# Kernel tuning notes

Measured on AMD Instinct MI355X. Metric: run time of the kernel, lower is better.

Reference implementation:

```python
import jax, jax.numpy as jnp
import numpy as np

OUT, IN = 4096, 4096
B, S = 2, 2048

def setup_inputs() -> dict:
    key = jax.random.key(0)
    k1, k2, k3, k4 = jax.random.split(key, 4)
    x = jax.random.normal(k1, (B, S, IN), dtype=jnp.float32)
    # symmetric int8 quantized weight [out, in]
    weight_q = jax.random.randint(k2, (OUT, IN), -128, 128, dtype=jnp.int32).astype(jnp.int8)
    # per-output-channel scale, small positive (like |w|_max/127)
    scale = (jax.random.uniform(k3, (1, OUT), dtype=jnp.float32) * 0.01 + 1e-4)
    bias = jax.random.normal(k4, (OUT,), dtype=jnp.float32)
    return {"x": x, "weight_q": weight_q, "scale": scale, "bias": bias}

def reference(x, weight_q, scale, bias):
    # out = (x_2d @ W_q^T (dequantized)) * scale + bias
    x2d = x.reshape(-1, x.shape[-1])                       # [B*S, in]
    w = weight_q.astype(x.dtype)                            # dequant cast [out, in]
    out = jnp.einsum('ni,oi->no', x2d, w) * scale           # [B*S, out] * [1, out]
    out = out.reshape(x.shape[:-1] + (out.shape[-1],))
    return out + bias
```

## Files before the change

kernel.cpp:

```cpp
#include <hip/hip_runtime.h>
#include <stdint.h>


#define M_DIM 4096
#define N_DIM 4096
#define K_DIM 4096
#define BM 128
#define BN 256
#define BK 32
#define KT_N (K_DIM / BK)
#define BUF_SHORTS 12288
#define A_OFF 0
#define B_OFF 4096

typedef _Float16 f16x8 __attribute__((ext_vector_type(8)));
typedef __bf16   bf16x8v __attribute__((ext_vector_type(8)));
typedef float    f32x4 __attribute__((ext_vector_type(4)));

__device__ __forceinline__ unsigned short f32_f16_bits(float f) {
    _Float16 h = (_Float16)f;
    return __builtin_bit_cast(unsigned short, h);
}

__device__ __forceinline__ void gld16(const unsigned short* g, unsigned short* l) {
    __builtin_amdgcn_global_load_lds(
        (const __attribute__((address_space(1))) unsigned int*)g,
        (__attribute__((address_space(3))) unsigned int*)l,
        16, 0, 0);
}

__global__ __launch_bounds__(256) void cvt_x_f16(const float* __restrict__ x,
                                                 unsigned short* __restrict__ AT) {
    const int b   = blockIdx.x;
    const int mi  = b >> 6;
    const int kt2 = b & 63;
    const int t   = threadIdx.x;
    const int r   = t & 127;
    const int kt  = kt2 * 2 + (t >> 7);

    const float* xp = x + (size_t)(mi * 128 + r) * K_DIM + kt * 32;
    unsigned short hh[32];
    #pragma unroll
    for (int j4 = 0; j4 < 8; ++j4) {
        float4 v = *(const float4*)(xp + j4 * 4);
        hh[j4*4+0] = f32_f16_bits(v.x);
        hh[j4*4+1] = f32_f16_bits(v.y);
        hh[j4*4+2] = f32_f16_bits(v.z);
        hh[j4*4+3] = f32_f16_bits(v.w);
    }
    unsigned short* o = AT + (size_t)(mi * KT_N + kt) * 4096 + r * 8;
    #pragma unroll
    for (int ks = 0; ks < 4; ++ks) {
        uint4 p;
        p.x = (unsigned)hh[ks*8+0] | ((unsigned)hh[ks*8+1] << 16);
        p.y = (unsigned)hh[ks*8+2] | ((unsigned)hh[ks*8+3] << 16);
        p.z = (unsigned)hh[ks*8+4] | ((unsigned)hh[ks*8+5] << 16);
        p.w = (unsigned)hh[ks*8+6] | ((unsigned)hh[ks*8+7] << 16);
        *(uint4*)(o + ks * 1024) = p;
    }
}

__global__ __launch_bounds__(256) void cvt_w_f16(const int* __restrict__ wq,
                                                 unsigned short* __restrict__ BT) {
    const int b  = blockIdx.x;
    const int ni = b >> 7;
    const int kt = b & 127;
    const int c  = threadIdx.x;

    const int* wp = wq + (size_t)(ni * 256 + c) * K_DIM + kt * 32;
    unsigned short bb[32];
    #pragma unroll
    for (int j4 = 0; j4 < 8; ++j4) {
        int4 v = *(const int4*)(wp + j4 * 4);
        bb[j4*4+0] = f32_f16_bits((float)v.x);
        bb[j4*4+1] = f32_f16_bits((float)v.y);
        bb[j4*4+2] = f32_f16_bits((float)v.z);
        bb[j4*4+3] = f32_f16_bits((float)v.w);
    }
    unsigned short* ob = BT + (size_t)(ni * KT_N + kt) * 8192 + c * 8;
    #pragma unroll
    for (int ks = 0; ks < 4; ++ks) {
        uint4 p;
        p.x = (unsigned)bb[ks*8+0] | ((unsigned)bb[ks*8+1] << 16);
        p.y = (unsigned)bb[ks*8+2] | ((unsigned)bb[ks*8+3] << 16);
        p.z = (unsigned)bb[ks*8+4] | ((unsigned)bb[ks*8+5] << 16);
        p.w = (unsigned)bb[ks*8+6] | ((unsigned)bb[ks*8+7] << 16);
        *(uint4*)(ob + ks * 2048) = p;
    }
}

__global__ __launch_bounds__(512, 2) void gemm_pipe(
    const unsigned short* __restrict__ AT,
    const unsigned short* __restrict__ BT,
    const float* __restrict__ scale, const float* __restrict__ bias,
    float* __restrict__ out)
{
    __shared__ unsigned short lds[3 * BUF_SHORTS];

    const int t    = threadIdx.x;
    const int lane = t & 63;
    const int wid  = t >> 6;
    const int wr   = wid >> 2;
    const int wc   = wid & 3;
    const int lr   = lane & 15;
    const int ksf  = lane >> 4;

    const int bid = blockIdx.x;
    const int swz = (bid & 7) * 64 + (bid >> 3);
    const int mi  = swz & 31;
    const int ni  = swz >> 5;

    const int lbA  = (t & ~63) * 8;
    const int lbB0 = (t & ~63) * 8;
    const int lbB1 = ((t + 512) & ~63) * 8;
    const unsigned short* gA = AT + (size_t)mi * KT_N * 4096 + t * 8;
    const unsigned short* gB = BT + (size_t)ni * KT_N * 8192;

#define STAGE(bufbase, kt) do { \
    gld16(gA + (size_t)(kt) * 4096,                  lds + (bufbase) + A_OFF + lbA); \
    gld16(gB + (size_t)(kt) * 8192 + t * 8,          lds + (bufbase) + B_OFF + lbB0); \
    gld16(gB + (size_t)(kt) * 8192 + (t + 512) * 8,  lds + (bufbase) + B_OFF + lbB1); \
} while (0)

    int offA[4], offB[4];
    #pragma unroll
    for (int m = 0; m < 4; ++m)
        offA[m] = A_OFF + (ksf * 128 + wr * 64 + m * 16 + lr) * 8;
    #pragma unroll
    for (int n = 0; n < 4; ++n)
        offB[n] = B_OFF + (ksf * 256 + wc * 64 + n * 16 + lr) * 8;

    f32x4 acc[4][4];
    #pragma unroll
    for (int m = 0; m < 4; ++m)
        #pragma unroll
        for (int n = 0; n < 4; ++n)
            acc[m][n] = (f32x4){0.f, 0.f, 0.f, 0.f};

    STAGE(0, 0);
    STAGE(BUF_SHORTS, 1);
    asm volatile("s_waitcnt vmcnt(3)" ::: "memory");
    __builtin_amdgcn_s_barrier();

    int curB = 0;
    int preB = 2 * BUF_SHORTS;

    for (int kt = 0; kt < KT_N; ++kt) {
        const unsigned short* Lb = lds + curB;

        f16x8 a4[4], b4[4];
        #pragma unroll
        for (int m = 0; m < 4; ++m) a4[m] = *(const f16x8*)(Lb + offA[m]);
        #pragma unroll
        for (int n = 0; n < 4; ++n) b4[n] = *(const f16x8*)(Lb + offB[n]);

        if (kt + 2 < KT_N) STAGE(preB, kt + 2);

        asm volatile("s_waitcnt lgkmcnt(0)" ::: "memory");
        __builtin_amdgcn_sched_barrier(0);
        __builtin_amdgcn_s_setprio(1);
        #pragma unroll
        for (int m = 0; m < 4; ++m)
            #pragma unroll
            for (int n = 0; n < 4; ++n)
                acc[m][n] = __builtin_amdgcn_mfma_f32_16x16x32_f16(a4[m], b4[n], acc[m][n], 0, 0, 0);
        __builtin_amdgcn_s_setprio(0);

        if (kt + 2 < KT_N) asm volatile("s_waitcnt vmcnt(3)" ::: "memory");
        else               asm volatile("s_waitcnt vmcnt(0)" ::: "memory");
        __builtin_amdgcn_s_barrier();

        curB = (curB == 2 * BUF_SHORTS) ? 0 : curB + BUF_SHORTS;
        preB = (preB == 2 * BUF_SHORTS) ? 0 : preB + BUF_SHORTS;
    }
#undef STAGE

    #pragma unroll
    for (int n = 0; n < 4; ++n) {
        const int col = ni * BN + wc * 64 + n * 16 + lr;
        const float sc = scale[col];
        const float bi = bias[col];
        #pragma unroll
        for (int m = 0; m < 4; ++m) {
            const int r0 = mi * BM + wr * 64 + m * 16 + ksf * 4;
            #pragma unroll
            for (int j = 0; j < 4; ++j)
                out[(size_t)(r0 + j) * N_DIM + col] = acc[m][n][j] * sc + bi;
        }
    }
}

__device__ __forceinline__ unsigned short f32_bf16_rne(float f) {
    unsigned u = __float_as_uint(f);
    u += 0x7FFFu + ((u >> 16) & 1u);
    return (unsigned short)(u >> 16);
}

__device__ __forceinline__ void cvt2(float a, float b, unsigned& hi2, unsigned& lo2) {
    unsigned short ha = f32_bf16_rne(a), hb = f32_bf16_rne(b);
    float fa = __uint_as_float((unsigned)ha << 16);
    float fb = __uint_as_float((unsigned)hb << 16);
    unsigned short la = f32_bf16_rne(a - fa), lb = f32_bf16_rne(b - fb);
    hi2 = (unsigned)ha | ((unsigned)hb << 16);
    lo2 = (unsigned)la | ((unsigned)lb << 16);
}

__global__ __launch_bounds__(256) void gemm_fb(
    const float* __restrict__ X, const int* __restrict__ Wq,
    const float* __restrict__ scale, const float* __restrict__ bias,
    float* __restrict__ out)
{
    __shared__ unsigned short sAh[4 * 128 * 8];
    __shared__ unsigned short sAl[4 * 128 * 8];
    __shared__ unsigned short sB [4 * 128 * 8];

    const int t    = threadIdx.x;
    const int lane = t & 63;
    const int wid  = t >> 6;
    const int brow = blockIdx.y * 128;
    const int bcol = blockIdx.x * 128;

    const int c1 = t,        c2 = t + 256;
    const int r1 = c1 & 127, s1 = c1 >> 7;
    const int r2 = c2 & 127, s2 = c2 >> 7;

    const int wr  = wid >> 1, wc = wid & 1;
    const int lr  = lane & 15;
    const int ksf = lane >> 4;

    f32x4 acc[4][4];
    #pragma unroll
    for (int m = 0; m < 4; ++m)
        #pragma unroll
        for (int n = 0; n < 4; ++n)
            acc[m][n] = (f32x4){0.f, 0.f, 0.f, 0.f};

    for (int k0 = 0; k0 < K_DIM; k0 += 32) {
        #pragma unroll
        for (int cc = 0; cc < 2; ++cc) {
            const int c = cc ? c2 : c1;
            const int r = cc ? r2 : r1;
            const int s = cc ? s2 : s1;
            const float* xa = X + (size_t)(brow + r) * K_DIM + k0 + s * 8;
            float4 v0 = *(const float4*)(xa);
            float4 v1 = *(const float4*)(xa + 4);
            uint4 hv, lv;
            cvt2(v0.x, v0.y, hv.x, lv.x);
            cvt2(v0.z, v0.w, hv.y, lv.y);
            cvt2(v1.x, v1.y, hv.z, lv.z);
            cvt2(v1.z, v1.w, hv.w, lv.w);
            *(uint4*)(sAh + c * 8) = hv;
            *(uint4*)(sAl + c * 8) = lv;

            const int* wa = Wq + (size_t)(bcol + r) * K_DIM + k0 + s * 8;
            int4 w0 = *(const int4*)(wa);
            int4 w1 = *(const int4*)(wa + 4);
            uint4 wv;
            wv.x = (unsigned)f32_bf16_rne((float)w0.x) | ((unsigned)f32_bf16_rne((float)w0.y) << 16);
            wv.y = (unsigned)f32_bf16_rne((float)w0.z) | ((unsigned)f32_bf16_rne((float)w0.w) << 16);
            wv.z = (unsigned)f32_bf16_rne((float)w1.x) | ((unsigned)f32_bf16_rne((float)w1.y) << 16);
            wv.w = (unsigned)f32_bf16_rne((float)w1.z) | ((unsigned)f32_bf16_rne((float)w1.w) << 16);
            *(uint4*)(sB + c * 8) = wv;
        }
        __syncthreads();

        bf16x8v ah[4], al[4], bb[4];
        #pragma unroll
        for (int m = 0; m < 4; ++m) {
            const int row = wr * 64 + m * 16 + lr;
            ah[m] = *(const bf16x8v*)(sAh + (ksf * 128 + row) * 8);
            al[m] = *(const bf16x8v*)(sAl + (ksf * 128 + row) * 8);
        }
        #pragma unroll
        for (int n = 0; n < 4; ++n) {
            const int row = wc * 64 + n * 16 + lr;
            bb[n] = *(const bf16x8v*)(sB + (ksf * 128 + row) * 8);
        }

        #pragma unroll
        for (int m = 0; m < 4; ++m)
            #pragma unroll
            for (int n = 0; n < 4; ++n) {
                acc[m][n] = __builtin_amdgcn_mfma_f32_16x16x32_bf16(ah[m], bb[n], acc[m][n], 0, 0, 0);
                acc[m][n] = __builtin_amdgcn_mfma_f32_16x16x32_bf16(al[m], bb[n], acc[m][n], 0, 0, 0);
            }
        __syncthreads();
    }

    #pragma unroll
    for (int n = 0; n < 4; ++n) {
        const int col = bcol + wc * 64 + n * 16 + lr;
        const float sc = scale[col];
        const float bi = bias[col];
        #pragma unroll
        for (int m = 0; m < 4; ++m) {
            const int r0 = brow + wr * 64 + m * 16 + ksf * 4;
            #pragma unroll
            for (int j = 0; j < 4; ++j)
                out[(size_t)(r0 + j) * N_DIM + col] = acc[m][n][j] * sc + bi;
        }
    }
}

extern "C" void kernel_launch(void* const* d_in, const int* in_sizes, int n_in,
                              void* d_out, int out_size, void* d_ws, size_t ws_size,
                              hipStream_t stream) {
    const float* x     = (const float*)d_in[0];
    const int*   wq    = (const int*)d_in[1];
    const float* scale = (const float*)d_in[2];
    const float* bias  = (const float*)d_in[3];
    float*       out   = (float*)d_out;

    const size_t planeElems = (size_t)M_DIM * K_DIM;
    const size_t planeBytes = planeElems * sizeof(unsigned short);

    if (ws_size >= 2 * planeBytes) {
        unsigned short* AT = (unsigned short*)d_ws;
        unsigned short* BT = AT + planeElems;
        cvt_x_f16<<<2048, 256, 0, stream>>>(x, AT);
        cvt_w_f16<<<2048, 256, 0, stream>>>(wq, BT);
        gemm_pipe<<<(M_DIM / BM) * (N_DIM / BN), 512, 0, stream>>>(AT, BT, scale, bias, out);
    } else {
        dim3 grid(N_DIM / 128, M_DIM / 128);
        gemm_fb<<<grid, 256, 0, stream>>>(x, wq, scale, bias, out);
    }
}
```

Measured before the change: 169.1 us.

## Enlarge GEMM block tile to 256x256 with uniform packed A/B tile layout

Doubles the M tile from 128 to 256 rows so each workgroup computes a 256x256 output tile. Each wave now does 8x4 MFMA tiles per K step, which reuses every B fragment across twice as many A fragments and halves the number of workgroups re-reading B. To support this, the f16 pre-pack of x now uses the same 8192-short tile layout as W, and the LDS staging issues four equal-sized global-to-LDS loads per stage. The cost is a doubled accumulator array, which puts heavy pressure on registers under launch_bounds(512,2), and a 96KB triple-buffered LDS footprint that likely allows only one workgroup per CU. It also depends on the host launching a grid that matches the new tile count.

```diff
diff --git a/kernel.cpp b/kernel.cpp
--- a/kernel.cpp
+++ b/kernel.cpp
@@ -5,13 +5,13 @@
 #define M_DIM 4096
 #define N_DIM 4096
 #define K_DIM 4096
-#define BM 128
+#define BM 256
 #define BN 256
 #define BK 32
 #define KT_N (K_DIM / BK)
-#define BUF_SHORTS 12288
-#define A_OFF 0
-#define B_OFF 4096
+#define TILE_SHORTS 8192
+#define BUF_SHORTS 16384
+#define B_OFF 8192
 
 typedef _Float16 f16x8 __attribute__((ext_vector_type(8)));
 typedef __bf16   bf16x8v __attribute__((ext_vector_type(8)));
@@ -31,14 +31,12 @@
 
 __global__ __launch_bounds__(256) void cvt_x_f16(const float* __restrict__ x,
                                                  unsigned short* __restrict__ AT) {
-    const int b   = blockIdx.x;
-    const int mi  = b >> 6;
-    const int kt2 = b & 63;
-    const int t   = threadIdx.x;
-    const int r   = t & 127;
-    const int kt  = kt2 * 2 + (t >> 7);
-
-    const float* xp = x + (size_t)(mi * 128 + r) * K_DIM + kt * 32;
+    const int b  = blockIdx.x;
+    const int mi = b >> 7;
+    const int kt = b & 127;
+    const int r  = threadIdx.x;
+
+    const float* xp = x + (size_t)(mi * 256 + r) * K_DIM + kt * 32;
     unsigned short hh[32];
     #pragma unroll
     for (int j4 = 0; j4 < 8; ++j4) {
@@ -48,7 +46,7 @@
         hh[j4*4+2] = f32_f16_bits(v.z);
         hh[j4*4+3] = f32_f16_bits(v.w);
     }
-    unsigned short* o = AT + (size_t)(mi * KT_N + kt) * 4096 + r * 8;
+    unsigned short* o = AT + (size_t)(mi * KT_N + kt) * TILE_SHORTS + r * 8;
     #pragma unroll
     for (int ks = 0; ks < 4; ++ks) {
         uint4 p;
@@ -56,7 +54,7 @@
         p.y = (unsigned)hh[ks*8+2] | ((unsigned)hh[ks*8+3] << 16);
         p.z = (unsigned)hh[ks*8+4] | ((unsigned)hh[ks*8+5] << 16);
         p.w = (unsigned)hh[ks*8+6] | ((unsigned)hh[ks*8+7] << 16);
-        *(uint4*)(o + ks * 1024) = p;
+        *(uint4*)(o + ks * 2048) = p;
     }
 }
 
@@ -77,7 +75,7 @@
         bb[j4*4+2] = f32_f16_bits((float)v.z);
         bb[j4*4+3] = f32_f16_bits((float)v.w);
     }
-    unsigned short* ob = BT + (size_t)(ni * KT_N + kt) * 8192 + c * 8;
+    unsigned short* ob = BT + (size_t)(ni * KT_N + kt) * TILE_SHORTS + c * 8;
     #pragma unroll
     for (int ks = 0; ks < 4; ++ks) {
         uint4 p;
@@ -106,40 +104,40 @@
     const int ksf  = lane >> 4;
 
     const int bid = blockIdx.x;
-    const int swz = (bid & 7) * 64 + (bid >> 3);
-    const int mi  = swz & 31;
-    const int ni  = swz >> 5;
-
-    const int lbA  = (t & ~63) * 8;
-    const int lbB0 = (t & ~63) * 8;
-    const int lbB1 = ((t + 512) & ~63) * 8;
-    const unsigned short* gA = AT + (size_t)mi * KT_N * 4096 + t * 8;
-    const unsigned short* gB = BT + (size_t)ni * KT_N * 8192;
+    const int swz = (bid & 7) * 32 + (bid >> 3);
+    const int mi  = swz & 15;
+    const int ni  = swz >> 4;
+
+    const int lb0 = (t & ~63) * 8;
+    const int lb1 = lb0 + 4096;
+    const unsigned short* gA = AT + (size_t)mi * KT_N * TILE_SHORTS + t * 8;
+    const unsigned short* gB = BT + (size_t)ni * KT_N * TILE_SHORTS + t * 8;
 
 #define STAGE(bufbase, kt) do { \
-    gld16(gA + (size_t)(kt) * 4096,                  lds + (bufbase) + A_OFF + lbA); \
-    gld16(gB + (size_t)(kt) * 8192 + t * 8,          lds + (bufbase) + B_OFF + lbB0); \
-    gld16(gB + (size_t)(kt) * 8192 + (t + 512) * 8,  lds + (bufbase) + B_OFF + lbB1); \
+    gld16(gA + (size_t)(kt) * TILE_SHORTS,        lds + (bufbase) + lb0); \
+    gld16(gA + (size_t)(kt) * TILE_SHORTS + 4096, lds + (bufbase) + lb1); \
+    gld16(gB + (size_t)(kt) * TILE_SHORTS,        lds + (bufbase) + B_OFF + lb0); \
+    gld16(gB + (size_t)(kt) * TILE_SHORTS + 4096, lds + (bufbase) + B_OFF + lb1); \
 } while (0)
 
-    int offA[4], offB[4];
-    #pragma unroll
-    for (int m = 0; m < 4; ++m)
-        offA[m] = A_OFF + (ksf * 128 + wr * 64 + m * 16 + lr) * 8;
+    int offA[8], offB[4];
+    #pragma unroll
+    for (int m = 0; m < 8; ++m)
+        offA[m] = (ksf * 256 + wr * 128 + m * 16 + lr) * 8;
     #pragma unroll
     for (int n = 0; n < 4; ++n)
         offB[n] = B_OFF + (ksf * 256 + wc * 64 + n * 16 + lr) * 8;
 
-    f32x4 acc[4][4];
-    #pragma unroll
-    for (int m = 0; m < 4; ++m)
+    f32x4 acc[8][4];
+    #pragma unroll
+    for (int m = 0; m < 8; ++m)
         #pragma unroll
         for (int n = 0; n < 4; ++n)
             acc[m][n] = (f32x4){0.f, 0.f, 0.f, 0.f};
 
     STAGE(0, 0);
     STAGE(BUF_SHORTS, 1);
-    asm volatile("s_waitcnt vmcnt(3)" ::: "memory");
+    asm volatile("s_waitcnt vmcnt(4)" ::: "memory");
     __builtin_amdgcn_s_barrier();
 
     int curB = 0;
@@ -148,9 +146,9 @@
     for (int kt = 0; kt < KT_N; ++kt) {
         const unsigned short* Lb = lds + curB;
 
-        f16x8 a4[4], b4[4];
-        #pragma unroll
-        for (int m = 0; m < 4; ++m) a4[m] = *(const f16x8*)(Lb + offA[m]);
+        f16x8 a4[8], b4[4];
+        #pragma unroll
+        for (int m = 0; m < 8; ++m) a4[m] = *(const f16x8*)(Lb + offA[m]);
         #pragma unroll
         for (int n = 0; n < 4; ++n) b4[n] = *(const f16x8*)(Lb + offB[n]);
 
@@ -160,13 +158,13 @@
         __builtin_amdgcn_sched_barrier(0);
         __builtin_amdgcn_s_setprio(1);
         #pragma unroll
-        for (int m = 0; m < 4; ++m)
+        for (int m = 0; m < 8; ++m)
             #pragma unroll
             for (int n = 0; n < 4; ++n)
                 acc[m][n] = __builtin_amdgcn_mfma_f32_16x16x32_f16(a4[m], b4[n], acc[m][n], 0, 0, 0);
         __builtin_amdgcn_s_setprio(0);
 
-        if (kt + 2 < KT_N) asm volatile("s_waitcnt vmcnt(3)" ::: "memory");
+        if (kt + 2 < KT_N) asm volatile("s_waitcnt vmcnt(4)" ::: "memory");
         else               asm volatile("s_waitcnt vmcnt(0)" ::: "memory");
         __builtin_amdgcn_s_barrier();
 
@@ -181,8 +179,8 @@
         const float sc = scale[col];
         const float bi = bias[col];
         #pragma unroll
-        for (int m = 0; m < 4; ++m) {
-            const int r0 = mi * BM + wr * 64 + m * 16 + ksf * 4;
+        for (int m = 0; m < 8; ++m) {
+            const int r0 = mi * BM + wr * 128 + m * 16 + ksf * 4;
             #pragma unroll
             for (int j = 0; j < 4; ++j)
                 out[(size_t)(r0 + j) * N_DIM + col] = acc[m][n][j] * sc + bi;
```

Result: faster. 160.1 us (-5.3%).
